# Performance work log

Hardware: AMD Instinct MI355X
Metric: run time of the kernel (lower is better)

The kernel has to match this reference:

```python
import jax, jax.numpy as jnp
import numpy as np

N_NODES = 32768
EMB_DIM = 128
N_CODES = 4096
N_GRAPHS = 512
ALPHA = 0.5            # args.alpha_init buffer
COMMIT_W = 1.0         # args.commitment_weight
BN_EPS = 1e-5


def setup_inputs() -> dict:
    key = jax.random.key(0)
    ks = jax.random.split(key, 8)
    node_feat = jax.random.normal(ks[0], (N_NODES, EMB_DIM), dtype=jnp.float32)
    score = jax.random.uniform(ks[1], (N_NODES, 1), dtype=jnp.float32)
    batch = jnp.sort(jax.random.randint(ks[2], (N_NODES,), 0, N_GRAPHS)).astype(jnp.int64)
    codebook_c = jax.random.normal(ks[3], (N_CODES, EMB_DIM), dtype=jnp.float32)
    codebook_s = jax.random.normal(ks[4], (N_CODES, EMB_DIM), dtype=jnp.float32)
    w1 = jax.random.normal(ks[5], (EMB_DIM, 2 * EMB_DIM), dtype=jnp.float32) * (1.0 / np.sqrt(EMB_DIM))
    b1 = jnp.zeros((2 * EMB_DIM,), dtype=jnp.float32)
    gamma = jnp.ones((2 * EMB_DIM,), dtype=jnp.float32)
    beta = jnp.zeros((2 * EMB_DIM,), dtype=jnp.float32)
    run_mean = jnp.zeros((2 * EMB_DIM,), dtype=jnp.float32)
    run_var = jnp.ones((2 * EMB_DIM,), dtype=jnp.float32)
    w2 = jax.random.normal(ks[6], (2 * EMB_DIM, 1), dtype=jnp.float32) * (1.0 / np.sqrt(2 * EMB_DIM))
    b2 = jnp.zeros((1,), dtype=jnp.float32)
    return {"node_feat": node_feat, "score": score, "batch": batch,
            "codebook_c": codebook_c, "codebook_s": codebook_s,
            "w1": w1, "b1": b1, "gamma": gamma, "beta": beta,
            "run_mean": run_mean, "run_var": run_var, "w2": w2, "b2": b2}


def _vector_quantize(x, codebook):
    # squared euclidean distance [N, K]; argmin lookup with straight-through.
    d2 = (jnp.sum(x * x, axis=-1, keepdims=True)
          - 2.0 * (x @ codebook.T)
          + jnp.sum(codebook * codebook, axis=-1))
    idx = jnp.argmin(d2, axis=-1)                     # [N]
    quantize = codebook[idx]                          # gather [N, D]
    commit_loss = jnp.mean((jax.lax.stop_gradient(quantize) - x) ** 2) * COMMIT_W
    out = x + jax.lax.stop_gradient(quantize - x)     # straight-through estimator
    return out, idx, commit_loss


def _mean_pool(x, batch):
    sums = jax.ops.segment_sum(x, batch, num_segments=N_GRAPHS)
    counts = jax.ops.segment_sum(jnp.ones((x.shape[0], 1), x.dtype), batch, num_segments=N_GRAPHS)
    return sums / jnp.maximum(counts, 1.0)


def reference(node_feat, score, batch, codebook_c, codebook_s,
              w1, b1, gamma, beta, run_mean, run_var, w2, b2):
    h_c = node_feat * score + ALPHA * node_feat * (1.0 - score)
    h_s = node_feat * (1.0 - score) + ALPHA * node_feat * score
    vq_c, _, cmt_loss_c = _vector_quantize(h_c, codebook_c)
    vq_s, _, cmt_loss_s = _vector_quantize(h_s, codebook_s)
    c_node_feat = node_feat * score + vq_c
    s_node_feat = node_feat * (1.0 - score) + vq_s
    c_graph_feat = _mean_pool(c_node_feat, batch)
    s_graph_feat = _mean_pool(s_node_feat, batch)
    # classifier: Linear -> BatchNorm1d (eval) -> ReLU -> Dropout(identity) -> Linear
    h = c_graph_feat @ w1 + b1
    h = (h - run_mean) * jax.lax.rsqrt(run_var + BN_EPS) * gamma + beta
    h = jax.nn.relu(h)
    c_logit = h @ w2 + b2
    return (c_logit, c_graph_feat, s_graph_feat, cmt_loss_c, cmt_loss_s, c_node_feat, s_node_feat)
```

## Files before the change

kernel.cpp:

```cpp
#include <hip/hip_runtime.h>
#include <hip/hip_bf16.h>

#define NODES   32768
#define DIM     128
#define NCODES  4096
#define NGRAPHS 512
#define THR     0.0625f

#define OFF_LOGIT 0
#define OFF_CG    512
#define OFF_SG    66048
#define OFF_LC    131584
#define OFF_LS    131585
#define OFF_CN    131586
#define OFF_SN    4325890

#define SPLIT_U16   263680
#define PLANE_U16   524288
#define HALF_F32    1180416
#define CSLOT_F32   1442560

#define WS_CNORM    0
#define WS_IDX      32768
#define WS_FLAGCNT  294928
#define WS_STARTS   294936
#define WS_FLAGLIST 296988
#define FLAG_CAP    32767

typedef __attribute__((ext_vector_type(8))) _Float16 f16x8_t;
typedef __attribute__((ext_vector_type(4))) float f32x4_t;

__device__ __forceinline__ float h_of(float x, float sc, int cb) {
    float omsc = __fsub_rn(1.0f, sc);
    float half_x = __fmul_rn(0.5f, x);
    if (cb == 0)
        return __fadd_rn(__fmul_rn(x, sc), __fmul_rn(half_x, omsc));
    else
        return __fadd_rn(__fmul_rn(x, omsc), __fmul_rn(half_x, sc));
}

__device__ __forceinline__ unsigned short f2h(float f) {
    return __builtin_bit_cast(unsigned short, (_Float16)f);
}

__device__ __forceinline__ void gload_lds16(const void* g, void* l) {
    __builtin_amdgcn_global_load_lds(
        (const __attribute__((address_space(1))) int*)g,
        (__attribute__((address_space(3))) int*)l, 16, 0, 0);
}

__device__ __forceinline__ unsigned sortkey(float f) {
    unsigned b = __float_as_uint(f);
    return (b & 0x80000000u) ? ~b : (b | 0x80000000u);
}
__device__ __forceinline__ float keyinv(unsigned k) {
    unsigned b = (k & 0x80000000u) ? (k & 0x7FFFFFFFu) : ~k;
    return __uint_as_float(b);
}

__global__ __launch_bounds__(256) void prep_kernel(
    const float* __restrict__ cb_c, const float* __restrict__ cb_s,
    const int* __restrict__ batch,
    float* __restrict__ cnorm, unsigned short* __restrict__ splits,
    int* __restrict__ starts, int* __restrict__ flagcnt)
{
    int gwave = (blockIdx.x * 256 + threadIdx.x) >> 6;
    int lane  = threadIdx.x & 63;

    if (gwave < 2 * NCODES) {
        int cb = gwave >> 12, row = gwave & (NCODES - 1);
        const float* cp = (cb ? cb_s : cb_c) + (size_t)row * DIM;
        float2 v = ((const float2*)cp)[lane];
        float p = __fadd_rn(__fmul_rn(v.x, v.x), __fmul_rn(v.y, v.y));
        #pragma unroll
        for (int off = 32; off; off >>= 1) p = __fadd_rn(p, __shfl_xor(p, off, 64));
        if (lane == 0) cnorm[cb * NCODES + row] = p;
        unsigned int* hp = (unsigned int*)(splits + (size_t)cb * PLANE_U16);
        hp[row * 64 + lane] = (unsigned)f2h(v.x) | ((unsigned)f2h(v.y) << 16);
    } else {
        int w1 = gwave - 2 * NCODES;
        int g = w1 * 64 + lane;
        if (g <= NGRAPHS) {
            int lo = 0, hi = NODES;
            while (lo < hi) { int mid = (lo + hi) >> 1; if (batch[mid] < g) lo = mid + 1; else hi = mid; }
            starts[g] = lo;
        }
        if (w1 == 0 && lane < 2) flagcnt[lane] = 0;
    }
}

__global__ __launch_bounds__(256, 2) void vq_main_kernel(
    const float* __restrict__ node_feat, const float* __restrict__ score,
    const unsigned short* __restrict__ splits, const float* __restrict__ cnorm,
    unsigned long long* __restrict__ halfres)
{
    __shared__ __align__(16) char lds[65536];
    const int nb    = blockIdx.x & 127;
    const int half  = blockIdx.x >> 7;
    const int cb    = blockIdx.y;
    const int nbase = nb * 256;
    const int tid = threadIdx.x;
    const int w   = tid >> 6;
    const int l15 = tid & 15;
    const int lg  = (tid & 63) >> 4;
    const int swz = (tid & 7) << 4;
    const float* cnp = cnorm + cb * NCODES + half * 2048;

    #pragma unroll
    for (int i = 0; i < 32; ++i) {
        int idx = i * 1024 + tid * 4;
        int row = idx >> 7, k = idx & 127;
        float4 x = *(const float4*)&node_feat[(size_t)(nbase + row) * DIM + k];
        float sc = score[nbase + row];
        unsigned u0 = f2h(h_of(x.x, sc, cb)), u1 = f2h(h_of(x.y, sc, cb));
        unsigned u2 = f2h(h_of(x.z, sc, cb)), u3 = f2h(h_of(x.w, sc, cb));
        int abyte = row * 256 + ((2 * k) ^ ((row & 7) << 4));
        uint2 hw; hw.x = u0 | (u1 << 16); hw.y = u2 | (u3 << 16);
        *(uint2*)(lds + abyte) = hw;
    }
    __syncthreads();

    f16x8_t ahi[4][4];
    int colbyte[4];
    #pragma unroll
    for (int ch = 0; ch < 4; ++ch) colbyte[ch] = (ch * 64 + lg * 16) ^ swz;
    #pragma unroll
    for (int rs = 0; rs < 4; ++rs)
        #pragma unroll
        for (int ch = 0; ch < 4; ++ch) {
            int row = 64 * w + 16 * rs + l15;
            ahi[rs][ch] = *(const f16x8_t*)(lds + row * 256 + colbyte[ch]);
        }
    __syncthreads();

    const unsigned short* wplane = splits + (size_t)cb * PLANE_U16 + half * 262144;
    int soff[4];
    #pragma unroll
    for (int i = 0; i < 4; ++i) {
        int row = w * 16 + i * 4 + lg;
        soff[i] = row * 256 + ((l15 * 16) ^ ((row & 7) << 4));
    }

    {
        const char* tb = (const char*)wplane;
        #pragma unroll
        for (int i = 0; i < 4; ++i)
            gload_lds16(tb + soff[i], lds + w * 4096 + i * 1024);
    }
    __syncthreads();

    const float NEG_INF = -3.4e38f;
    float b1v[4][4], b2v[4][4]; int b1i[4][4];
    #pragma unroll
    for (int rs = 0; rs < 4; ++rs)
        #pragma unroll
        for (int r = 0; r < 4; ++r) { b1v[rs][r] = NEG_INF; b2v[rs][r] = NEG_INF; b1i[rs][r] = 0; }

    for (int t = 0; t < 32; ++t) {
        int bs_cur = (t & 1) << 14;
        float cnc[4];
        #pragma unroll
        for (int cs = 0; cs < 4; ++cs) cnc[cs] = __fmul_rn(-0.5f, cnp[t * 64 + cs * 16 + l15]);
        if (t < 31) {
            int bs_nxt = ((t + 1) & 1) << 14;
            const char* tb = (const char*)wplane + (t + 1) * 16384;
            #pragma unroll
            for (int i = 0; i < 4; ++i)
                gload_lds16(tb + soff[i], lds + bs_nxt + w * 4096 + i * 1024);
        }

        #pragma unroll
        for (int cp = 0; cp < 2; ++cp) {
            f32x4_t acc[4][2];
            #pragma unroll
            for (int rs = 0; rs < 4; ++rs)
                #pragma unroll
                for (int c2 = 0; c2 < 2; ++c2) {
                    float iv = cnc[cp * 2 + c2];
                    acc[rs][c2] = (f32x4_t){iv, iv, iv, iv};
                }

            #pragma unroll
            for (int ch = 0; ch < 4; ++ch)
                #pragma unroll
                for (int c2 = 0; c2 < 2; ++c2) {
                    int cs = cp * 2 + c2;
                    f16x8_t bh = *(const f16x8_t*)(lds + bs_cur +
                                                   (cs * 16 + l15) * 256 + colbyte[ch]);
                    #pragma unroll
                    for (int rs = 0; rs < 4; ++rs)
                        acc[rs][c2] = __builtin_amdgcn_mfma_f32_16x16x32_f16(ahi[rs][ch], bh, acc[rs][c2], 0, 0, 0);
                }

            #pragma unroll
            for (int c2 = 0; c2 < 2; ++c2) {
                int cs = cp * 2 + c2;
                int code = half * 2048 + t * 64 + cs * 16 + l15;
                #pragma unroll
                for (int rs = 0; rs < 4; ++rs)
                    #pragma unroll
                    for (int r = 0; r < 4; ++r) {
                        float a = acc[rs][c2][r];
                        bool gt = a > b1v[rs][r];
                        float nb2 = __builtin_amdgcn_fmed3f(a, b1v[rs][r], b2v[rs][r]);
                        if (gt) b1i[rs][r] = code;
                        b1v[rs][r] = fmaxf(a, b1v[rs][r]);
                        b2v[rs][r] = nb2;
                    }
            }
        }
        __syncthreads();
    }

    #pragma unroll
    for (int off = 1; off < 16; off <<= 1) {
        #pragma unroll
        for (int rs = 0; rs < 4; ++rs)
            #pragma unroll
            for (int r = 0; r < 4; ++r) {
                float ov1 = __shfl_xor(b1v[rs][r], off, 64);
                int   oi  = __shfl_xor(b1i[rs][r], off, 64);
                float ov2 = __shfl_xor(b2v[rs][r], off, 64);
                bool take = (ov1 > b1v[rs][r]) || (ov1 == b1v[rs][r] && oi < b1i[rs][r]);
                float loser = fminf(ov1, b1v[rs][r]);
                b1v[rs][r] = fmaxf(ov1, b1v[rs][r]);
                if (take) b1i[rs][r] = oi;
                b2v[rs][r] = fmaxf(loser, fmaxf(ov2, b2v[rs][r]));
            }
    }
    if (l15 == 0) {
        #pragma unroll
        for (int rs = 0; rs < 4; ++rs)
            #pragma unroll
            for (int r = 0; r < 4; ++r) {
                int node = nbase + 64 * w + 16 * rs + 4 * lg + r;
                unsigned key = sortkey(b1v[rs][r]);
                unsigned pay = (unsigned)b1i[rs][r] |
                               ((b1v[rs][r] - b2v[rs][r] < THR) ? 0x1000u : 0u);
                halfres[((size_t)(cb * 2 + half)) * NODES + node] =
                    ((unsigned long long)key << 32) | pay;
            }
    }
}

__global__ __launch_bounds__(256) void resolve_kernel(
    const unsigned long long* __restrict__ hr, unsigned long long* __restrict__ cslot,
    int* __restrict__ idx_ws, int* __restrict__ flagcnt, int* __restrict__ flaglist)
{
    int cb = blockIdx.y;
    int node = blockIdx.x * 256 + threadIdx.x;
    unsigned long long A = hr[((size_t)(cb * 2 + 0)) * NODES + node];
    unsigned long long B = hr[((size_t)(cb * 2 + 1)) * NODES + node];
    unsigned ka = (unsigned)(A >> 32), kb = (unsigned)(B >> 32);
    bool awin = ka >= kb;
    unsigned long long W = awin ? A : B;
    float aw = keyinv(awin ? ka : kb);
    float al = keyinv(awin ? kb : ka);
    bool flag = ((W >> 12) & 1ull) || (__fsub_rn(aw, al) < THR);
    idx_ws[cb * NODES + node] = (int)(W & 0xFFFu);
    if (flag) cslot[(size_t)cb * NODES + node] = ~0ull;

    unsigned long long mask = __ballot(flag);
    if (mask) {
        int lane = threadIdx.x & 63;
        int leader = __ffsll((long long)mask) - 1;
        int base = 0;
        if (lane == leader) base = atomicAdd(flagcnt + cb, (int)__popcll(mask));
        base = __shfl(base, leader, 64);
        if (flag) {
            int pos = base + (int)__popcll(mask & ((1ull << lane) - 1ull));
            if (pos < FLAG_CAP) flaglist[cb * FLAG_CAP + pos] = node;
        }
    }
}

__global__ __launch_bounds__(256) void vq_cleanup_kernel(
    const float* __restrict__ node_feat, const float* __restrict__ score,
    const float* __restrict__ cb_c, const float* __restrict__ cb_s,
    const float* __restrict__ cnorm, const int* __restrict__ flagcnt,
    const int* __restrict__ flaglist, unsigned long long* __restrict__ slots)
{
    __shared__ char cbS[32768];
    __shared__ float hbuf[8][128];
    const int cb  = blockIdx.y;
    const int seg = blockIdx.x & 63;
    const int ng  = blockIdx.x >> 6;
    const float* cbp = cb ? cb_s : cb_c;
    const int* list = flaglist + cb * FLAG_CAP;
    int cnt = flagcnt[cb]; if (cnt > FLAG_CAP) cnt = FLAG_CAP;
    const int tid = threadIdx.x, w = tid >> 6, l = tid & 63;

    {
        int c = tid >> 2, ks = (tid & 3) * 32;
        const float* src = cbp + (size_t)(seg * 64 + c) * DIM + ks;
        char* dst = cbS + c * 512;
        int sw = (c & 7) << 4;
        #pragma unroll
        for (int j = 0; j < 8; ++j) {
            float4 v = *(const float4*)(src + j * 4);
            *(float4*)(dst + ((ks * 4 + j * 16) ^ sw)) = v;
        }
    }
    const int mycode = seg * 64 + l;
    const float cn = cnorm[cb * NCODES + mycode];
    const int swl = (l & 7) << 4;
    const char* crow = cbS + l * 512;
    __syncthreads();

    for (int base = ng * 8; base < cnt; base += 512) {
        int eA = base + 2 * w, eB = eA + 1;
        bool vA = eA < cnt, vB = eB < cnt;
        int nA = list[vA ? eA : 0], nB = list[vB ? eB : 0];
        float scA = score[nA], scB = score[nB];
        float a0 = h_of(node_feat[(size_t)nA * DIM + l],      scA, cb);
        float a1 = h_of(node_feat[(size_t)nA * DIM + 64 + l], scA, cb);
        float b0 = h_of(node_feat[(size_t)nB * DIM + l],      scB, cb);
        float b1 = h_of(node_feat[(size_t)nB * DIM + 64 + l], scB, cb);
        hbuf[2 * w][l] = a0;     hbuf[2 * w][64 + l] = a1;
        hbuf[2 * w + 1][l] = b0; hbuf[2 * w + 1][64 + l] = b1;
        float sxA = __fadd_rn(__fmul_rn(a0, a0), __fmul_rn(a1, a1));
        float sxB = __fadd_rn(__fmul_rn(b0, b0), __fmul_rn(b1, b1));
        #pragma unroll
        for (int off = 32; off; off >>= 1) {
            sxA = __fadd_rn(sxA, __shfl_xor(sxA, off, 64));
            sxB = __fadd_rn(sxB, __shfl_xor(sxB, off, 64));
        }
        asm volatile("s_waitcnt lgkmcnt(0)" ::: "memory");

        float pA0 = 0.f, pA1 = 0.f, pA2 = 0.f, pA3 = 0.f;
        float pB0 = 0.f, pB1 = 0.f, pB2 = 0.f, pB3 = 0.f;
        const float4* hA = (const float4*)hbuf[2 * w];
        const float4* hB = (const float4*)hbuf[2 * w + 1];
        #pragma unroll 8
        for (int m = 0; m < 32; ++m) {
            float4 c4 = *(const float4*)(crow + ((m * 16) ^ swl));
            float4 ha = hA[m], hb = hB[m];
            pA0 = fmaf(ha.x, c4.x, pA0); pA1 = fmaf(ha.y, c4.y, pA1);
            pA2 = fmaf(ha.z, c4.z, pA2); pA3 = fmaf(ha.w, c4.w, pA3);
            pB0 = fmaf(hb.x, c4.x, pB0); pB1 = fmaf(hb.y, c4.y, pB1);
            pB2 = fmaf(hb.z, c4.z, pB2); pB3 = fmaf(hb.w, c4.w, pB3);
        }
        float dotA = __fadd_rn(__fadd_rn(pA0, pA1), __fadd_rn(pA2, pA3));
        float dotB = __fadd_rn(__fadd_rn(pB0, pB1), __fadd_rn(pB2, pB3));
        float dA = __fadd_rn(__fsub_rn(sxA, __fmul_rn(2.0f, dotA)), cn);
        float dB = __fadd_rn(__fsub_rn(sxB, __fmul_rn(2.0f, dotB)), cn);

        unsigned long long pkA = ((unsigned long long)sortkey(dA) << 32) | (unsigned)mycode;
        unsigned long long pkB = ((unsigned long long)sortkey(dB) << 32) | (unsigned)mycode;
        #pragma unroll
        for (int off = 1; off < 64; off <<= 1) {
            unsigned long long oA = __shfl_xor(pkA, off, 64);
            unsigned long long oB = __shfl_xor(pkB, off, 64);
            pkA = (oA < pkA) ? oA : pkA;
            pkB = (oB < pkB) ? oB : pkB;
        }
        if (l == 0 && vA) atomicMin(&slots[(size_t)cb * NODES + nA], pkA);
        if (l == 0 && vB) atomicMin(&slots[(size_t)cb * NODES + nB], pkB);
        asm volatile("s_waitcnt lgkmcnt(0)" ::: "memory");
    }
}

__global__ __launch_bounds__(256) void flag_writeback_kernel(
    const int* __restrict__ flagcnt, const int* __restrict__ flaglist,
    const unsigned long long* __restrict__ slots, int* __restrict__ idx_ws)
{
    int gt = blockIdx.x * 256 + threadIdx.x;
    int c0 = flagcnt[0]; if (c0 > FLAG_CAP) c0 = FLAG_CAP;
    int c1 = flagcnt[1]; if (c1 > FLAG_CAP) c1 = FLAG_CAP;
    for (int e = gt; e < 2 * FLAG_CAP; e += 256 * 256) {
        int cb = (e >= FLAG_CAP) ? 1 : 0;
        int i = e - cb * FLAG_CAP;
        int cnt = cb ? c1 : c0;
        if (i < cnt) {
            int node = flaglist[cb * FLAG_CAP + i];
            idx_ws[cb * NODES + node] =
                (int)(slots[(size_t)cb * NODES + node] & 0xFFFFFFFFull);
        }
    }
}

__global__ __launch_bounds__(256) void gather_kernel(
    const float* __restrict__ node_feat, const float* __restrict__ score,
    const float* __restrict__ cb_c, const float* __restrict__ cb_s,
    const int* __restrict__ idx_all, float* __restrict__ out,
    double* __restrict__ partials)
{
    __shared__ float redc[4], reds[4];
    int wave = threadIdx.x >> 6, lane = threadIdx.x & 63;
    int node = blockIdx.x * 4 + wave;
    float sc = score[node];
    float2 x  = *(const float2*)&node_feat[(size_t)node * DIM + 2 * lane];
    int ic = idx_all[node], is_ = idx_all[NODES + node];
    float2 qc = *(const float2*)&cb_c[(size_t)ic * DIM + 2 * lane];
    float2 qs = *(const float2*)&cb_s[(size_t)is_ * DIM + 2 * lane];

    float omsc = __fsub_rn(1.0f, sc);
    float2 cn, sn;
    cn.x = __fadd_rn(__fmul_rn(x.x, sc), qc.x);
    cn.y = __fadd_rn(__fmul_rn(x.y, sc), qc.y);
    sn.x = __fadd_rn(__fmul_rn(x.x, omsc), qs.x);
    sn.y = __fadd_rn(__fmul_rn(x.y, omsc), qs.y);
    *(float2*)&out[OFF_CN + (size_t)node * DIM + 2 * lane] = cn;
    *(float2*)&out[OFF_SN + (size_t)node * DIM + 2 * lane] = sn;

    float hc1 = h_of(x.x, sc, 0), hc2 = h_of(x.y, sc, 0);
    float hs1 = h_of(x.x, sc, 1), hs2 = h_of(x.y, sc, 1);
    float d1 = qc.x - hc1, d2 = qc.y - hc2;
    float e1 = qs.x - hs1, e2 = qs.y - hs2;
    float lc = d1 * d1 + d2 * d2;
    float ls = e1 * e1 + e2 * e2;
    #pragma unroll
    for (int off = 32; off; off >>= 1) {
        lc += __shfl_down(lc, off, 64);
        ls += __shfl_down(ls, off, 64);
    }
    if (lane == 0) { redc[wave] = lc; reds[wave] = ls; }
    __syncthreads();
    if (threadIdx.x == 0) {
        partials[blockIdx.x]        = (double)redc[0] + redc[1] + redc[2] + redc[3];
        partials[8192 + blockIdx.x] = (double)reds[0] + reds[1] + reds[2] + reds[3];
    }
}

__global__ __launch_bounds__(256) void loss_reduce_kernel(
    const double* __restrict__ partials, float* __restrict__ out)
{
    __shared__ double red[4];
    int b = blockIdx.x, t = threadIdx.x, w = t >> 6, l = t & 63;
    const double* p = partials + b * 8192;
    double s = 0.0;
    #pragma unroll 4
    for (int i = t; i < 8192; i += 256) s += p[i];
    #pragma unroll
    for (int off = 32; off; off >>= 1) s += __shfl_down(s, off, 64);
    if (l == 0) red[w] = s;
    __syncthreads();
    if (t == 0) {
        double tot = (red[0] + red[1]) + (red[2] + red[3]);
        out[OFF_LC + b] = (float)(tot * (1.0 / 4194304.0));
    }
}

__global__ __launch_bounds__(512) void pool_kernel(
    const int* __restrict__ starts, float* __restrict__ out)
{
    __shared__ float part[4][128];
    int g = blockIdx.x, half = blockIdx.y;
    int d = threadIdx.x & 127, nl = threadIdx.x >> 7;
    int s = starts[g], e = starts[g + 1];
    const float* src = out + (half ? OFF_SN : OFF_CN);
    float sum = 0.0f;
    for (int n = s + nl; n < e; n += 4) sum = __fadd_rn(sum, src[(size_t)n * DIM + d]);
    part[nl][d] = sum;
    __syncthreads();
    if (nl == 0) {
        float tot = __fadd_rn(__fadd_rn(part[0][d], part[1][d]),
                              __fadd_rn(part[2][d], part[3][d]));
        float cnt = fmaxf((float)(e - s), 1.0f);
        out[(half ? OFF_SG : OFF_CG) + g * DIM + d] = __fdiv_rn(tot, cnt);
    }
}

__global__ __launch_bounds__(256) void classifier_kernel(
    const float* __restrict__ w1, const float* __restrict__ b1,
    const float* __restrict__ gamma, const float* __restrict__ beta,
    const float* __restrict__ rm, const float* __restrict__ rv,
    const float* __restrict__ w2, const float* __restrict__ b2,
    float* __restrict__ out)
{
    __shared__ float row[DIM];
    __shared__ float red[4];
    int g = blockIdx.x, t = threadIdx.x;
    if (t < DIM) row[t] = out[OFF_CG + g * DIM + t];
    __syncthreads();
    float h = 0.0f;
    #pragma unroll 8
    for (int k = 0; k < DIM; ++k) h = fmaf(row[k], w1[k * 256 + t], h);
    h = __fadd_rn(h, b1[t]);
    float inv = __frsqrt_rn(__fadd_rn(rv[t], 1e-5f));
    h = __fadd_rn(__fmul_rn(__fmul_rn(__fsub_rn(h, rm[t]), inv), gamma[t]), beta[t]);
    h = fmaxf(h, 0.0f);
    float p = __fmul_rn(h, w2[t]);
    #pragma unroll
    for (int off = 32; off; off >>= 1) p += __shfl_down(p, off, 64);
    if ((t & 63) == 0) red[t >> 6] = p;
    __syncthreads();
    if (t == 0) {
        float total = __fadd_rn(__fadd_rn(red[0], red[1]), __fadd_rn(red[2], red[3]));
        out[OFF_LOGIT + g] = __fadd_rn(total, b2[0]);
    }
}

extern "C" void kernel_launch(void* const* d_in, const int* in_sizes, int n_in,
                              void* d_out, int out_size, void* d_ws, size_t ws_size,
                              hipStream_t stream) {
    const float* node_feat = (const float*)d_in[0];
    const float* score     = (const float*)d_in[1];
    const int*   batch     = (const int*)d_in[2];
    const float* cb_c      = (const float*)d_in[3];
    const float* cb_s      = (const float*)d_in[4];
    const float* w1        = (const float*)d_in[5];
    const float* b1        = (const float*)d_in[6];
    const float* gamma     = (const float*)d_in[7];
    const float* beta      = (const float*)d_in[8];
    const float* rm        = (const float*)d_in[9];
    const float* rv        = (const float*)d_in[10];
    const float* w2        = (const float*)d_in[11];
    const float* b2        = (const float*)d_in[12];
    float* out = (float*)d_out;
    char*  ws  = (char*)d_ws;

    float*  cnorm    = (float*)(ws + WS_CNORM);
    int*    idx      = (int*)(ws + WS_IDX);
    int*    flagcnt  = (int*)(ws + WS_FLAGCNT);
    int*    starts   = (int*)(ws + WS_STARTS);
    int*    flaglist = (int*)(ws + WS_FLAGLIST);
    unsigned short* splits = (unsigned short*)d_out + SPLIT_U16;
    unsigned long long* halfres = (unsigned long long*)(out + HALF_F32);
    unsigned long long* cslot   = (unsigned long long*)(out + CSLOT_F32);
    double* partials = (double*)(out + OFF_CG);

    prep_kernel<<<2051, 256, 0, stream>>>(cb_c, cb_s, batch, cnorm, splits,
                                          starts, flagcnt);
    vq_main_kernel<<<dim3(256, 2), 256, 0, stream>>>(node_feat, score, splits, cnorm,
                                                     halfres);
    resolve_kernel<<<dim3(128, 2), 256, 0, stream>>>(halfres, cslot, idx,
                                                     flagcnt, flaglist);
    vq_cleanup_kernel<<<dim3(4096, 2), 256, 0, stream>>>(node_feat, score, cb_c, cb_s,
                                                         cnorm, flagcnt, flaglist, cslot);
    flag_writeback_kernel<<<256, 256, 0, stream>>>(flagcnt, flaglist, cslot, idx);
    gather_kernel<<<8192, 256, 0, stream>>>(node_feat, score, cb_c, cb_s, idx, out, partials);
    loss_reduce_kernel<<<2, 256, 0, stream>>>(partials, out);
    pool_kernel<<<dim3(512, 2), 512, 0, stream>>>(starts, out);
    classifier_kernel<<<512, 256, 0, stream>>>(w1, b1, gamma, beta, rm, rv, w2, b2, out);
}
```

Before: 323.8 us.

## Pre-swizzle codebook into fragment order and triple-buffer codebook tiles in LDS

The prep kernel now writes the fp16 codebook directly in MFMA B-fragment order, so the main kernel's async global-to-LDS loads and LDS reads become contiguous per lane with no XOR swizzle. The main loop switches from double buffering with a full __syncthreads each iteration to a three-slot ring with two tiles in flight, using explicit vmcnt waits and a single s_barrier. Code norms are staged once into LDS, pre-scaled by -0.5, instead of read from global memory every iteration. The aim is to hide codebook load latency and cut address arithmetic and bank conflicts, at the cost of more LDS use and hand-written wait counts that must stay exactly right.

Result: faster. 315.5 us (-2.6%).

```diff
diff --git a/kernel.cpp b/kernel.cpp
--- a/kernel.cpp
+++ b/kernel.cpp
@@ -68,15 +68,20 @@
     int lane  = threadIdx.x & 63;
 
     if (gwave < 2 * NCODES) {
-        int cb = gwave >> 12, row = gwave & (NCODES - 1);
-        const float* cp = (cb ? cb_s : cb_c) + (size_t)row * DIM;
+        int cb = gwave >> 12, code = gwave & (NCODES - 1);
+        const float* cp = (cb ? cb_s : cb_c) + (size_t)code * DIM;
         float2 v = ((const float2*)cp)[lane];
         float p = __fadd_rn(__fmul_rn(v.x, v.x), __fmul_rn(v.y, v.y));
         #pragma unroll
         for (int off = 32; off; off >>= 1) p = __fadd_rn(p, __shfl_xor(p, off, 64));
-        if (lane == 0) cnorm[cb * NCODES + row] = p;
+        if (lane == 0) cnorm[cb * NCODES + code] = p;
+
+        int hf = code >> 11, tt = (code >> 6) & 31, cs = (code >> 4) & 3, l15c = code & 15;
+        int ch = lane >> 4, lg = (lane >> 2) & 3, jw = lane & 3;
         unsigned int* hp = (unsigned int*)(splits + (size_t)cb * PLANE_U16);
-        hp[row * 64 + lane] = (unsigned)f2h(v.x) | ((unsigned)f2h(v.y) << 16);
+        int u32idx = hf * 131072 +
+                     ((tt * 16 + cs * 4 + ch) * 64 + lg * 16 + l15c) * 4 + jw;
+        hp[u32idx] = (unsigned)f2h(v.x) | ((unsigned)f2h(v.y) << 16);
     } else {
         int w1 = gwave - 2 * NCODES;
         int g = w1 * 64 + lane;
@@ -99,12 +104,12 @@
     const int half  = blockIdx.x >> 7;
     const int cb    = blockIdx.y;
     const int nbase = nb * 256;
-    const int tid = threadIdx.x;
-    const int w   = tid >> 6;
-    const int l15 = tid & 15;
-    const int lg  = (tid & 63) >> 4;
-    const int swz = (tid & 7) << 4;
-    const float* cnp = cnorm + cb * NCODES + half * 2048;
+    const int tid  = threadIdx.x;
+    const int w    = tid >> 6;
+    const int lane = tid & 63;
+    const int l15  = tid & 15;
+    const int lg   = lane >> 4;
+    const int swz  = (tid & 7) << 4;
 
     #pragma unroll
     for (int i = 0; i < 32; ++i) {
@@ -133,21 +138,27 @@
         }
     __syncthreads();
 
-    const unsigned short* wplane = splits + (size_t)cb * PLANE_U16 + half * 262144;
-    int soff[4];
-    #pragma unroll
-    for (int i = 0; i < 4; ++i) {
-        int row = w * 16 + i * 4 + lg;
-        soff[i] = row * 256 + ((l15 * 16) ^ ((row & 7) << 4));
-    }
-
     {
-        const char* tb = (const char*)wplane;
-        #pragma unroll
-        for (int i = 0; i < 4; ++i)
-            gload_lds16(tb + soff[i], lds + w * 4096 + i * 1024);
-    }
-    __syncthreads();
+        const float* cnp = cnorm + cb * NCODES + half * 2048;
+        float4 v0 = *(const float4*)&cnp[tid * 8];
+        float4 v1 = *(const float4*)&cnp[tid * 8 + 4];
+        float4 n0 = {__fmul_rn(-0.5f, v0.x), __fmul_rn(-0.5f, v0.y),
+                     __fmul_rn(-0.5f, v0.z), __fmul_rn(-0.5f, v0.w)};
+        float4 n1 = {__fmul_rn(-0.5f, v1.x), __fmul_rn(-0.5f, v1.y),
+                     __fmul_rn(-0.5f, v1.z), __fmul_rn(-0.5f, v1.w)};
+        *(float4*)(lds + 49152 + tid * 32) = n0;
+        *(float4*)(lds + 49152 + tid * 32 + 16) = n1;
+    }
+
+    const char* planeB = (const char*)(splits + (size_t)cb * PLANE_U16 + half * 262144);
+    const char* gsrc = planeB + w * 4096 + lane * 16;
+    #pragma unroll
+    for (int i = 0; i < 4; ++i)
+        gload_lds16(gsrc + i * 1024, lds + w * 4096 + i * 1024);
+    #pragma unroll
+    for (int i = 0; i < 4; ++i)
+        gload_lds16(gsrc + 16384 + i * 1024, lds + 16384 + w * 4096 + i * 1024);
+    asm volatile("s_waitcnt lgkmcnt(0)" ::: "memory");
 
     const float NEG_INF = -3.4e38f;
     float b1v[4][4], b2v[4][4]; int b1i[4][4];
@@ -157,59 +168,49 @@
         for (int r = 0; r < 4; ++r) { b1v[rs][r] = NEG_INF; b2v[rs][r] = NEG_INF; b1i[rs][r] = 0; }
 
     for (int t = 0; t < 32; ++t) {
-        int bs_cur = (t & 1) << 14;
-        float cnc[4];
-        #pragma unroll
-        for (int cs = 0; cs < 4; ++cs) cnc[cs] = __fmul_rn(-0.5f, cnp[t * 64 + cs * 16 + l15]);
-        if (t < 31) {
-            int bs_nxt = ((t + 1) & 1) << 14;
-            const char* tb = (const char*)wplane + (t + 1) * 16384;
+        if (t < 31) { asm volatile("s_waitcnt vmcnt(4)" ::: "memory"); }
+        else        { asm volatile("s_waitcnt vmcnt(0)" ::: "memory"); }
+        __builtin_amdgcn_s_barrier();
+        __builtin_amdgcn_sched_barrier(0);
+
+        if (t < 30) {
+            int onx = ((t + 2) % 3) * 16384;
+            const char* ts = planeB + (t + 2) * 16384 + w * 4096 + lane * 16;
+            char* td = lds + onx + w * 4096;
             #pragma unroll
             for (int i = 0; i < 4; ++i)
-                gload_lds16(tb + soff[i], lds + bs_nxt + w * 4096 + i * 1024);
-        }
-
-        #pragma unroll
-        for (int cp = 0; cp < 2; ++cp) {
-            f32x4_t acc[4][2];
+                gload_lds16(ts + i * 1024, td + i * 1024);
+        }
+
+        const char* bufc = lds + (t % 3) * 16384;
+        #pragma unroll
+        for (int cs = 0; cs < 4; ++cs) {
+            float cnc = *(const float*)(lds + 49152 + ((t * 64 + cs * 16 + l15) << 2));
+            f32x4_t acc[4];
+            #pragma unroll
+            for (int rs = 0; rs < 4; ++rs) acc[rs] = (f32x4_t){cnc, cnc, cnc, cnc};
+
+            #pragma unroll
+            for (int ch = 0; ch < 4; ++ch) {
+                f16x8_t bh = *(const f16x8_t*)(bufc + (cs * 4 + ch) * 1024 + lane * 16);
+                #pragma unroll
+                for (int rs = 0; rs < 4; ++rs)
+                    acc[rs] = __builtin_amdgcn_mfma_f32_16x16x32_f16(ahi[rs][ch], bh, acc[rs], 0, 0, 0);
+            }
+
+            int code = half * 2048 + t * 64 + cs * 16 + l15;
             #pragma unroll
             for (int rs = 0; rs < 4; ++rs)
                 #pragma unroll
-                for (int c2 = 0; c2 < 2; ++c2) {
-                    float iv = cnc[cp * 2 + c2];
-                    acc[rs][c2] = (f32x4_t){iv, iv, iv, iv};
+                for (int r = 0; r < 4; ++r) {
+                    float a = acc[rs][r];
+                    bool gt = a > b1v[rs][r];
+                    float nb2 = __builtin_amdgcn_fmed3f(a, b1v[rs][r], b2v[rs][r]);
+                    if (gt) b1i[rs][r] = code;
+                    b1v[rs][r] = fmaxf(a, b1v[rs][r]);
+                    b2v[rs][r] = nb2;
                 }
-
-            #pragma unroll
-            for (int ch = 0; ch < 4; ++ch)
-                #pragma unroll
-                for (int c2 = 0; c2 < 2; ++c2) {
-                    int cs = cp * 2 + c2;
-                    f16x8_t bh = *(const f16x8_t*)(lds + bs_cur +
-                                                   (cs * 16 + l15) * 256 + colbyte[ch]);
-                    #pragma unroll
-                    for (int rs = 0; rs < 4; ++rs)
-                        acc[rs][c2] = __builtin_amdgcn_mfma_f32_16x16x32_f16(ahi[rs][ch], bh, acc[rs][c2], 0, 0, 0);
-                }
-
-            #pragma unroll
-            for (int c2 = 0; c2 < 2; ++c2) {
-                int cs = cp * 2 + c2;
-                int code = half * 2048 + t * 64 + cs * 16 + l15;
-                #pragma unroll
-                for (int rs = 0; rs < 4; ++rs)
-                    #pragma unroll
-                    for (int r = 0; r < 4; ++r) {
-                        float a = acc[rs][c2][r];
-                        bool gt = a > b1v[rs][r];
-                        float nb2 = __builtin_amdgcn_fmed3f(a, b1v[rs][r], b2v[rs][r]);
-                        if (gt) b1i[rs][r] = code;
-                        b1v[rs][r] = fmaxf(a, b1v[rs][r]);
-                        b2v[rs][r] = nb2;
-                    }
-            }
-        }
-        __syncthreads();
+        }
     }
 
     #pragma unroll
```
